# Kernel optimization log

Measured on AMD Instinct MI355X. Metric: run time of the kernel, lower is better.

## Reference

```python
import jax, jax.numpy as jnp
import numpy as np

N_NODES = 100000
N_EDGES = 1200000
N_HOP = 3
DIM = 64
EPS = 1e-5


def _bn(x):
    # BatchNorm1d over nodes, train-mode stats, gamma=1, beta=0
    m = x.mean(axis=0)
    v = x.var(axis=0)
    return (x - m) / jnp.sqrt(v + EPS)


def _gcn_conv(x, W, b, src, dst, n):
    # PyG GCNConv: add self-loops, symmetric deg^-1/2 (A+I) deg^-1/2, then bias
    xw = x @ W                                            # [N, D]
    deg = jax.ops.segment_sum(jnp.ones_like(src, dtype=xw.dtype), dst,
                              num_segments=n) + 1.0       # self-loop adds 1
    dinv = jax.lax.rsqrt(deg)                             # deg >= 1
    coef = dinv[src] * dinv[dst]                          # [E]
    agg = jax.ops.segment_sum(xw[src] * coef[:, None], dst, num_segments=n)
    agg = agg + (dinv * dinv)[:, None] * xw               # self-loop message
    return agg + b


def setup_inputs() -> dict:
    key = jax.random.key(0)
    ks = jax.random.split(key, 8)
    backbone_outputs = jax.random.normal(ks[0], (4, N_NODES, DIM), dtype=jnp.float32)
    khop_edge_index = jax.random.randint(ks[1], (N_HOP, 2, N_EDGES), 0, N_NODES)
    comb_w = jax.random.normal(ks[2], (N_HOP + 1, 3), dtype=jnp.float32)
    ego_W = jax.random.normal(ks[3], (DIM, DIM), dtype=jnp.float32) / np.sqrt(DIM)
    ego_b = jnp.zeros((DIM,), dtype=jnp.float32)
    conv_W = jax.random.normal(ks[4], (N_HOP, DIM, DIM), dtype=jnp.float32) / np.sqrt(DIM)
    conv_b = jnp.zeros((N_HOP, DIM), dtype=jnp.float32)
    return {"backbone_outputs": backbone_outputs, "comb_w": comb_w,
            "ego_W": ego_W, "ego_b": ego_b, "conv_W": conv_W, "conv_b": conv_b,
            "khop_edge_index": khop_edge_index}


def reference(backbone_outputs, comb_w, ego_W, ego_b, conv_W, conv_b, khop_edge_index):
    n = backbone_outputs.shape[1]
    # SimpleCombine: softmax-weighted mixes of backbone layer outputs (skip input)
    w = jax.nn.softmax(comb_w, axis=1)                    # [n_hop+1, 3]
    multi = jnp.einsum('ji,ind->jnd', w, backbone_outputs[1:])  # [n_hop+1, N, D]
    # ego path: linear -> BN (dropout=0)
    hidden = _bn(multi[0] @ ego_W + ego_b)
    for k in range(N_HOP):
        src = khop_edge_index[k, 0]
        dst = khop_edge_index[k, 1]
        prop = _gcn_conv(multi[k + 1], conv_W[k], conv_b[k], src, dst, n)
        hidden = hidden + jax.nn.relu(_bn(prop))
    return jax.nn.log_softmax(hidden, axis=1)
```

## Files before the change

### kernel.cpp

```cpp
#include <hip/hip_runtime.h>
#include <hip/hip_bf16.h>

#define NND 100000
#define NED 1200000
#define NHOP 3
#define DM 64
#define EPSV 1e-5f
#define NB1 391

typedef long long i64;
typedef unsigned short u16;
typedef unsigned int u32;

__device__ __forceinline__ float rlf(float v, int k) {
    return __builtin_bit_cast(float, __builtin_amdgcn_readlane(__builtin_bit_cast(int, v), k));
}
__device__ __forceinline__ float bf2f(u16 b) {
    return __builtin_bit_cast(float, (u32)b << 16);
}
__device__ __forceinline__ u16 f2bf(float f) {
    u32 u = __builtin_bit_cast(u32, f);
    return (u16)((u + 0x7FFFu + ((u >> 16) & 1u)) >> 16);
}

__global__ void k_weights(const float* __restrict__ comb_w, float* __restrict__ wsoft) {
    int j = threadIdx.x;
    if (j < NHOP + 1) {
        float a0 = comb_w[j * 3 + 0], a1 = comb_w[j * 3 + 1], a2 = comb_w[j * 3 + 2];
        float mx = fmaxf(a0, fmaxf(a1, a2));
        float e0 = expf(a0 - mx), e1 = expf(a1 - mx), e2 = expf(a2 - mx);
        float s = 1.0f / (e0 + e1 + e2);
        wsoft[j * 3 + 0] = e0 * s; wsoft[j * 3 + 1] = e1 * s; wsoft[j * 3 + 2] = e2 * s;
    }
}

__global__ __launch_bounds__(256) void k_gemm(const float* __restrict__ bb,
                                              const float* __restrict__ wsoft, int j,
                                              const float* __restrict__ W,
                                              const float* __restrict__ dinv, int scale,
                                              float* __restrict__ stats, int dostats,
                                              u16* __restrict__ xw) {
    const int lane = threadIdx.x & 63;
    float Wcol[DM];
#pragma unroll
    for (int k = 0; k < DM; k++) Wcol[k] = W[k * DM + lane];
    const float w0 = wsoft[j * 3 + 0], w1 = wsoft[j * 3 + 1], w2 = wsoft[j * 3 + 2];
    const float* b1 = bb + (i64)1 * NND * DM;
    const float* b2 = bb + (i64)2 * NND * DM;
    const float* b3 = bb + (i64)3 * NND * DM;
    int wave = (int)((blockIdx.x * blockDim.x + threadIdx.x) >> 6);
    int nw = (int)((gridDim.x * blockDim.x) >> 6);
    float s = 0.f, sq = 0.f;
    for (int n = wave; n < NND; n += nw) {
        i64 base = (i64)n * DM + lane;
        float m = w0 * b1[base] + w1 * b2[base] + w2 * b3[base];
        float a0 = 0.f, a1 = 0.f, a2 = 0.f, a3 = 0.f;
#pragma unroll
        for (int k = 0; k < DM; k += 4) {
            a0 = fmaf(rlf(m, k + 0), Wcol[k + 0], a0);
            a1 = fmaf(rlf(m, k + 1), Wcol[k + 1], a1);
            a2 = fmaf(rlf(m, k + 2), Wcol[k + 2], a2);
            a3 = fmaf(rlf(m, k + 3), Wcol[k + 3], a3);
        }
        float r = (a0 + a1) + (a2 + a3);
        if (scale) r *= dinv[n];
        xw[base] = f2bf(r);
        s += r; sq += r * r;
    }
    if (dostats) {
        __shared__ float ls[4][DM], lq[4][DM];
        int row = threadIdx.x >> 6;
        ls[row][lane] = s; lq[row][lane] = sq;
        __syncthreads();
        if (row == 0) {
            s  = ls[0][lane] + ls[1][lane] + ls[2][lane] + ls[3][lane];
            sq = lq[0][lane] + lq[1][lane] + lq[2][lane] + lq[3][lane];
            unsafeAtomicAdd(&stats[lane], s);
            unsafeAtomicAdd(&stats[DM + lane], sq);
        }
    }
}

__global__ __launch_bounds__(256) void k_deg(const int* __restrict__ dst, int* __restrict__ deg) {
    int i = blockIdx.x * blockDim.x + threadIdx.x;
    int stride = gridDim.x * blockDim.x;
    for (int e = i; e < NED; e += stride) atomicAdd(&deg[dst[e]], 1);
}

__global__ __launch_bounds__(256) void k_scan1(const int* __restrict__ deg,
                                               int* __restrict__ off,
                                               int* __restrict__ partials,
                                               float* __restrict__ dinv) {
    int t = threadIdx.x;
    int n = blockIdx.x * 256 + t;
    int d = (n < NND) ? deg[n] : 0;
    if (n < NND) dinv[n] = rsqrtf((float)d + 1.0f);
    __shared__ int sh[256];
    sh[t] = d;
    __syncthreads();
    for (int o = 1; o < 256; o <<= 1) {
        int v = (t >= o) ? sh[t - o] : 0;
        __syncthreads();
        sh[t] += v;
        __syncthreads();
    }
    if (n < NND) off[n] = sh[t] - d;
    if (t == 255) partials[blockIdx.x] = sh[255];
}

__global__ __launch_bounds__(512) void k_scan2(int* __restrict__ partials) {
    int t = threadIdx.x;
    int d = (t < NB1) ? partials[t] : 0;
    __shared__ int sh[512];
    sh[t] = d;
    __syncthreads();
    for (int o = 1; o < 512; o <<= 1) {
        int v = (t >= o) ? sh[t - o] : 0;
        __syncthreads();
        sh[t] += v;
        __syncthreads();
    }
    if (t < NB1) partials[t] = sh[t] - d;
}

__global__ __launch_bounds__(256) void k_bucket(const int* __restrict__ src,
                                                const int* __restrict__ dst,
                                                int* __restrict__ off,
                                                const int* __restrict__ partials,
                                                int* __restrict__ sortedsrc) {
    int i = blockIdx.x * blockDim.x + threadIdx.x;
    int stride = gridDim.x * blockDim.x;
    for (int e = i; e < NED; e += stride) {
        int d = dst[e];
        int pos = partials[d >> 8] + atomicAdd(&off[d], 1);
        sortedsrc[pos] = src[e];
    }
}

__global__ __launch_bounds__(256) void k_gather(const u16* __restrict__ xws,
                                                const int* __restrict__ sortedsrc,
                                                const int* __restrict__ off,
                                                const int* __restrict__ partials,
                                                const int* __restrict__ deg,
                                                const float* __restrict__ dinv,
                                                float* __restrict__ xbuf,
                                                float* __restrict__ stats) {
    const int lane = threadIdx.x & 63;
    int wave = (int)((blockIdx.x * blockDim.x + threadIdx.x) >> 6);
    int nw = (int)((gridDim.x * blockDim.x) >> 6);
    float s = 0.f, sq = 0.f;
    for (int n = wave; n < NND; n += nw) {
        int cnt = deg[n];
        int start = partials[n >> 8] + off[n] - cnt;
        float acc = bf2f(xws[(i64)n * DM + lane]);
        int i = 0;
        while (i < cnt) {
            int m = cnt - i; if (m > 64) m = 64;
            int sl = (lane < m) ? sortedsrc[start + i + lane] : 0;
            int t = 0;
            for (; t + 4 <= m; t += 4) {
                int s0 = __builtin_amdgcn_readlane(sl, t + 0);
                int s1 = __builtin_amdgcn_readlane(sl, t + 1);
                int s2 = __builtin_amdgcn_readlane(sl, t + 2);
                int s3 = __builtin_amdgcn_readlane(sl, t + 3);
                float v0 = bf2f(xws[(i64)s0 * DM + lane]);
                float v1 = bf2f(xws[(i64)s1 * DM + lane]);
                float v2 = bf2f(xws[(i64)s2 * DM + lane]);
                float v3 = bf2f(xws[(i64)s3 * DM + lane]);
                acc += ((v0 + v1) + (v2 + v3));
            }
            for (; t < m; t++) {
                int ss = __builtin_amdgcn_readlane(sl, t);
                acc += bf2f(xws[(i64)ss * DM + lane]);
            }
            i += m;
        }
        float x = acc * dinv[n];
        xbuf[(i64)n * DM + lane] = x;
        s += x; sq += x * x;
    }
    __shared__ float ls[4][DM], lq[4][DM];
    int row = threadIdx.x >> 6;
    ls[row][lane] = s; lq[row][lane] = sq;
    __syncthreads();
    if (row == 0) {
        s  = ls[0][lane] + ls[1][lane] + ls[2][lane] + ls[3][lane];
        sq = lq[0][lane] + lq[1][lane] + lq[2][lane] + lq[3][lane];
        unsafeAtomicAdd(&stats[lane], s);
        unsafeAtomicAdd(&stats[DM + lane], sq);
    }
}

__global__ __launch_bounds__(256) void k_apply(const float* __restrict__ xbuf,
                                               const u16* __restrict__ xwsA, int mode,
                                               const float* __restrict__ statsA,
                                               const float* __restrict__ statsB,
                                               float* __restrict__ hidden,
                                               float* __restrict__ out) {
    const int lane = threadIdx.x & 63;
    float meanB = statsB[lane] * (1.0f / NND);
    float varB = statsB[DM + lane] * (1.0f / NND) - meanB * meanB;
    float invB = rsqrtf(varB + EPSV);
    float meanA = 0.f, invA = 0.f;
    if (mode == 0) {
        meanA = statsA[lane] * (1.0f / NND);
        float varA = statsA[DM + lane] * (1.0f / NND) - meanA * meanA;
        invA = rsqrtf(varA + EPSV);
    }
    int wave = (int)((blockIdx.x * blockDim.x + threadIdx.x) >> 6);
    int nw = (int)((gridDim.x * blockDim.x) >> 6);
    for (int n = wave; n < NND; n += nw) {
        i64 i = (i64)n * DM + lane;
        float bn = (xbuf[i] - meanB) * invB;
        float r = fmaxf(bn, 0.0f);
        if (mode == 0) {
            hidden[i] = (bf2f(xwsA[i]) - meanA) * invA + r;
        } else if (mode == 1) {
            hidden[i] += r;
        } else {
            float h = hidden[i] + r;
            float mx = h;
#pragma unroll
            for (int o = 32; o >= 1; o >>= 1) mx = fmaxf(mx, __shfl_xor(mx, o));
            float e = expf(h - mx);
            float ssum = e;
#pragma unroll
            for (int o = 32; o >= 1; o >>= 1) ssum += __shfl_xor(ssum, o);
            out[i] = h - mx - logf(ssum);
        }
    }
}

extern "C" void kernel_launch(void* const* d_in, const int* in_sizes, int n_in,
                              void* d_out, int out_size, void* d_ws, size_t ws_size,
                              hipStream_t stream) {
    const float* bb     = (const float*)d_in[0];
    const float* comb_w = (const float*)d_in[1];
    const float* ego_W  = (const float*)d_in[2];
    const float* conv_W = (const float*)d_in[4];
    const int*   edges  = (const int*)d_in[6];
    float* out = (float*)d_out;

    const i64 NF = (i64)NND * DM;
    char* ws = (char*)d_ws;
    float* wsoft     = (float*)ws;
    float* stats     = wsoft + 64;
    u16*   xwsA      = (u16*)(stats + 512);
    u16*   xwsB      = xwsA + NF;
    float* xbuf      = (float*)(xwsB + NF);
    float* dinv      = xbuf + NF;
    int*   deg       = (int*)(dinv + NND);
    int*   off       = deg + NND;
    int*   partials  = off + NND;
    int*   sortedsrc = partials + 512;
    float* hidden = out;

    k_weights<<<1, 64, 0, stream>>>(comb_w, wsoft);
    hipMemsetAsync(stats, 0, 4 * 128 * sizeof(float), stream);

    k_gemm<<<1024, 256, 0, stream>>>(bb, wsoft, 0, ego_W, dinv, 0, stats, 1, xwsA);

    for (int k = 0; k < NHOP; k++) {
        const int* src = edges + (i64)k * 2 * NED;
        const int* dst = src + NED;
        float* statsB = stats + (k + 1) * 128;
        hipMemsetAsync(deg, 0, NND * sizeof(int), stream);
        k_deg<<<1024, 256, 0, stream>>>(dst, deg);
        k_scan1<<<NB1, 256, 0, stream>>>(deg, off, partials, dinv);
        k_scan2<<<1, 512, 0, stream>>>(partials);
        k_gemm<<<1024, 256, 0, stream>>>(bb, wsoft, k + 1, conv_W + (i64)k * DM * DM,
                                         dinv, 1, statsB, 0, xwsB);
        k_bucket<<<1024, 256, 0, stream>>>(src, dst, off, partials, sortedsrc);
        k_gather<<<4096, 256, 0, stream>>>(xwsB, sortedsrc, off, partials, deg, dinv,
                                           xbuf, statsB);
        k_apply<<<512, 256, 0, stream>>>(xbuf, xwsA, k, stats, statsB, hidden, out);
    }
}
```

Baseline: 1.087 ms.

## Batch CSR build across hops and vectorize bf16 gather with 8-lane groups

Builds the CSR for all three hops in one batch: a combined degree count, scan, rowptr finalize and bucket pass, instead of a separate sequence per hop. The softmax weights and the dinv scaling are now computed inline, which drops the weights kernel and the dinv array. The gather now loads each neighbor row as 16-byte uint4 bf16 vectors, with 8 groups of 8 lanes each handling a different neighbor, then reduces across groups with shuffles. The intermediate xbuf is stored in bf16 instead of fp32, which halves its traffic in the apply kernel at the cost of extra rounding before BatchNorm. Launch sizes are also changed.

```diff
diff --git a/kernel.cpp b/kernel.cpp
--- a/kernel.cpp
+++ b/kernel.cpp
@@ -22,29 +22,24 @@
     u32 u = __builtin_bit_cast(u32, f);
     return (u16)((u + 0x7FFFu + ((u >> 16) & 1u)) >> 16);
 }
-
-__global__ void k_weights(const float* __restrict__ comb_w, float* __restrict__ wsoft) {
-    int j = threadIdx.x;
-    if (j < NHOP + 1) {
-        float a0 = comb_w[j * 3 + 0], a1 = comb_w[j * 3 + 1], a2 = comb_w[j * 3 + 2];
-        float mx = fmaxf(a0, fmaxf(a1, a2));
-        float e0 = expf(a0 - mx), e1 = expf(a1 - mx), e2 = expf(a2 - mx);
-        float s = 1.0f / (e0 + e1 + e2);
-        wsoft[j * 3 + 0] = e0 * s; wsoft[j * 3 + 1] = e1 * s; wsoft[j * 3 + 2] = e2 * s;
-    }
-}
+__device__ __forceinline__ float lo_f(u32 w) { return __builtin_bit_cast(float, w << 16); }
+__device__ __forceinline__ float hi_f(u32 w) { return __builtin_bit_cast(float, w & 0xFFFF0000u); }
 
 __global__ __launch_bounds__(256) void k_gemm(const float* __restrict__ bb,
-                                              const float* __restrict__ wsoft, int j,
+                                              const float* __restrict__ comb_w, int j,
                                               const float* __restrict__ W,
-                                              const float* __restrict__ dinv, int scale,
+                                              const int* __restrict__ rowptr, int scale,
                                               float* __restrict__ stats, int dostats,
                                               u16* __restrict__ xw) {
     const int lane = threadIdx.x & 63;
     float Wcol[DM];
 #pragma unroll
     for (int k = 0; k < DM; k++) Wcol[k] = W[k * DM + lane];
-    const float w0 = wsoft[j * 3 + 0], w1 = wsoft[j * 3 + 1], w2 = wsoft[j * 3 + 2];
+    float c0 = comb_w[j * 3 + 0], c1 = comb_w[j * 3 + 1], c2 = comb_w[j * 3 + 2];
+    float mx = fmaxf(c0, fmaxf(c1, c2));
+    float e0 = expf(c0 - mx), e1 = expf(c1 - mx), e2 = expf(c2 - mx);
+    float es = 1.0f / (e0 + e1 + e2);
+    const float w0 = e0 * es, w1 = e1 * es, w2 = e2 * es;
     const float* b1 = bb + (i64)1 * NND * DM;
     const float* b2 = bb + (i64)2 * NND * DM;
     const float* b3 = bb + (i64)3 * NND * DM;
@@ -63,7 +58,10 @@
             a3 = fmaf(rlf(m, k + 3), Wcol[k + 3], a3);
         }
         float r = (a0 + a1) + (a2 + a3);
-        if (scale) r *= dinv[n];
+        if (scale) {
+            int rs = rowptr[n], re = rowptr[n + 1];
+            r *= rsqrtf((float)(re - rs) + 1.0f);
+        }
         xw[base] = f2bf(r);
         s += r; sq += r * r;
     }
@@ -81,20 +79,26 @@
     }
 }
 
-__global__ __launch_bounds__(256) void k_deg(const int* __restrict__ dst, int* __restrict__ deg) {
+__global__ __launch_bounds__(256) void k_deg3(const int* __restrict__ edges, int* __restrict__ deg) {
     int i = blockIdx.x * blockDim.x + threadIdx.x;
     int stride = gridDim.x * blockDim.x;
-    for (int e = i; e < NED; e += stride) atomicAdd(&deg[dst[e]], 1);
+    for (int e = i; e < NED; e += stride) {
+#pragma unroll
+        for (int h = 0; h < NHOP; h++) {
+            int d = edges[(i64)h * 2 * NED + NED + e];
+            atomicAdd(&deg[h * NND + d], 1);
+        }
+    }
 }
 
 __global__ __launch_bounds__(256) void k_scan1(const int* __restrict__ deg,
-                                               int* __restrict__ off,
-                                               int* __restrict__ partials,
-                                               float* __restrict__ dinv) {
+                                               int* __restrict__ loc,
+                                               int* __restrict__ partials) {
     int t = threadIdx.x;
-    int n = blockIdx.x * 256 + t;
-    int d = (n < NND) ? deg[n] : 0;
-    if (n < NND) dinv[n] = rsqrtf((float)d + 1.0f);
+    int h = blockIdx.x / NB1;
+    int lb = blockIdx.x - h * NB1;
+    int n = lb * 256 + t;
+    int d = (n < NND) ? deg[h * NND + n] : 0;
     __shared__ int sh[256];
     sh[t] = d;
     __syncthreads();
@@ -104,13 +108,14 @@
         sh[t] += v;
         __syncthreads();
     }
-    if (n < NND) off[n] = sh[t] - d;
-    if (t == 255) partials[blockIdx.x] = sh[255];
+    if (n < NND) loc[h * NND + n] = sh[t] - d;
+    if (t == 255) partials[h * 512 + lb] = sh[255];
 }
 
 __global__ __launch_bounds__(512) void k_scan2(int* __restrict__ partials) {
     int t = threadIdx.x;
-    int d = (t < NB1) ? partials[t] : 0;
+    int h = blockIdx.x;
+    int d = (t < NB1) ? partials[h * 512 + t] : 0;
     __shared__ int sh[512];
     sh[t] = d;
     __syncthreads();
@@ -120,78 +125,128 @@
         sh[t] += v;
         __syncthreads();
     }
-    if (t < NB1) partials[t] = sh[t] - d;
-}
-
-__global__ __launch_bounds__(256) void k_bucket(const int* __restrict__ src,
-                                                const int* __restrict__ dst,
-                                                int* __restrict__ off,
-                                                const int* __restrict__ partials,
-                                                int* __restrict__ sortedsrc) {
+    if (t < NB1) partials[h * 512 + t] = sh[t] - d;
+}
+
+__global__ __launch_bounds__(256) void k_fin(const int* __restrict__ loc,
+                                             const int* __restrict__ partials,
+                                             int* __restrict__ rowptr,
+                                             int* __restrict__ cursor) {
+    int i = blockIdx.x * blockDim.x + threadIdx.x;
+    if (i >= NHOP * (NND + 1)) return;
+    int h = i / (NND + 1);
+    int n = i - h * (NND + 1);
+    int v;
+    if (n == NND) v = NED;
+    else v = partials[h * 512 + (n >> 8)] + loc[h * NND + n];
+    rowptr[h * (NND + 1) + n] = v;
+    if (n < NND) cursor[h * NND + n] = v;
+}
+
+__global__ __launch_bounds__(256) void k_bucket3(const int* __restrict__ edges,
+                                                 int* __restrict__ cursor,
+                                                 int* __restrict__ sortedsrc) {
     int i = blockIdx.x * blockDim.x + threadIdx.x;
     int stride = gridDim.x * blockDim.x;
     for (int e = i; e < NED; e += stride) {
-        int d = dst[e];
-        int pos = partials[d >> 8] + atomicAdd(&off[d], 1);
-        sortedsrc[pos] = src[e];
+#pragma unroll
+        for (int h = 0; h < NHOP; h++) {
+            int s = edges[(i64)h * 2 * NED + e];
+            int d = edges[(i64)h * 2 * NED + NED + e];
+            int pos = atomicAdd(&cursor[h * NND + d], 1);
+            sortedsrc[(i64)h * NED + pos] = s;
+        }
     }
 }
 
 __global__ __launch_bounds__(256) void k_gather(const u16* __restrict__ xws,
-                                                const int* __restrict__ sortedsrc,
-                                                const int* __restrict__ off,
-                                                const int* __restrict__ partials,
-                                                const int* __restrict__ deg,
-                                                const float* __restrict__ dinv,
-                                                float* __restrict__ xbuf,
+                                                const int* __restrict__ sorted,
+                                                const int* __restrict__ rowptr,
+                                                u16* __restrict__ xbuf,
                                                 float* __restrict__ stats) {
     const int lane = threadIdx.x & 63;
+    const int g = lane >> 3;
+    const int c = lane & 7;
+    const int wv = threadIdx.x >> 6;
     int wave = (int)((blockIdx.x * blockDim.x + threadIdx.x) >> 6);
     int nw = (int)((gridDim.x * blockDim.x) >> 6);
-    float s = 0.f, sq = 0.f;
+    float sA[8] = {0,0,0,0,0,0,0,0}, qA[8] = {0,0,0,0,0,0,0,0};
     for (int n = wave; n < NND; n += nw) {
-        int cnt = deg[n];
-        int start = partials[n >> 8] + off[n] - cnt;
-        float acc = bf2f(xws[(i64)n * DM + lane]);
-        int i = 0;
-        while (i < cnt) {
-            int m = cnt - i; if (m > 64) m = 64;
-            int sl = (lane < m) ? sortedsrc[start + i + lane] : 0;
-            int t = 0;
-            for (; t + 4 <= m; t += 4) {
-                int s0 = __builtin_amdgcn_readlane(sl, t + 0);
-                int s1 = __builtin_amdgcn_readlane(sl, t + 1);
-                int s2 = __builtin_amdgcn_readlane(sl, t + 2);
-                int s3 = __builtin_amdgcn_readlane(sl, t + 3);
-                float v0 = bf2f(xws[(i64)s0 * DM + lane]);
-                float v1 = bf2f(xws[(i64)s1 * DM + lane]);
-                float v2 = bf2f(xws[(i64)s2 * DM + lane]);
-                float v3 = bf2f(xws[(i64)s3 * DM + lane]);
-                acc += ((v0 + v1) + (v2 + v3));
+        int start = rowptr[n];
+        int cnt = rowptr[n + 1] - start;
+        uint4 sv = *(const uint4*)(xws + (i64)n * DM + c * 8);
+        float selfw = (g == 0) ? 1.0f : 0.0f;
+        float acc[8];
+        acc[0] = lo_f(sv.x) * selfw; acc[1] = hi_f(sv.x) * selfw;
+        acc[2] = lo_f(sv.y) * selfw; acc[3] = hi_f(sv.y) * selfw;
+        acc[4] = lo_f(sv.z) * selfw; acc[5] = hi_f(sv.z) * selfw;
+        acc[6] = lo_f(sv.w) * selfw; acc[7] = hi_f(sv.w) * selfw;
+        int base = 0;
+        while (base < cnt) {
+            int take = cnt - base; if (take > 64) take = 64;
+            int eidx = start + base + lane;
+            if (eidx > NED - 1) eidx = NED - 1;
+            int sli = sorted[eidx];
+            int nr = (take + 7) >> 3;
+            for (int r = 0; r < nr; r += 2) {
+                int i0 = r * 8 + g;
+                int i1 = i0 + 8;
+                int s0 = __shfl(sli, i0);
+                int s1 = __shfl(sli, i1 & 63);
+                uint4 v0 = *(const uint4*)(xws + (i64)s0 * DM + c * 8);
+                uint4 v1 = *(const uint4*)(xws + (i64)s1 * DM + c * 8);
+                float m0 = (i0 < take) ? 1.0f : 0.0f;
+                float m1 = (i1 < take) ? 1.0f : 0.0f;
+                acc[0] = fmaf(lo_f(v0.x), m0, acc[0]); acc[1] = fmaf(hi_f(v0.x), m0, acc[1]);
+                acc[2] = fmaf(lo_f(v0.y), m0, acc[2]); acc[3] = fmaf(hi_f(v0.y), m0, acc[3]);
+                acc[4] = fmaf(lo_f(v0.z), m0, acc[4]); acc[5] = fmaf(hi_f(v0.z), m0, acc[5]);
+                acc[6] = fmaf(lo_f(v0.w), m0, acc[6]); acc[7] = fmaf(hi_f(v0.w), m0, acc[7]);
+                acc[0] = fmaf(lo_f(v1.x), m1, acc[0]); acc[1] = fmaf(hi_f(v1.x), m1, acc[1]);
+                acc[2] = fmaf(lo_f(v1.y), m1, acc[2]); acc[3] = fmaf(hi_f(v1.y), m1, acc[3]);
+                acc[4] = fmaf(lo_f(v1.z), m1, acc[4]); acc[5] = fmaf(hi_f(v1.z), m1, acc[5]);
+                acc[6] = fmaf(lo_f(v1.w), m1, acc[6]); acc[7] = fmaf(hi_f(v1.w), m1, acc[7]);
             }
-            for (; t < m; t++) {
-                int ss = __builtin_amdgcn_readlane(sl, t);
-                acc += bf2f(xws[(i64)ss * DM + lane]);
-            }
-            i += m;
-        }
-        float x = acc * dinv[n];
-        xbuf[(i64)n * DM + lane] = x;
-        s += x; sq += x * x;
-    }
-    __shared__ float ls[4][DM], lq[4][DM];
-    int row = threadIdx.x >> 6;
-    ls[row][lane] = s; lq[row][lane] = sq;
+            base += take;
+        }
+        float dinv = rsqrtf((float)cnt + 1.0f);
+#pragma unroll
+        for (int i = 0; i < 8; i++) {
+            float v = acc[i];
+            v += __shfl_xor(v, 8);
+            v += __shfl_xor(v, 16);
+            v += __shfl_xor(v, 32);
+            float x = v * dinv;
+            acc[i] = x;
+            sA[i] += x; qA[i] += x * x;
+        }
+        if (g == 0) {
+            uint4 o;
+            o.x = (u32)f2bf(acc[0]) | ((u32)f2bf(acc[1]) << 16);
+            o.y = (u32)f2bf(acc[2]) | ((u32)f2bf(acc[3]) << 16);
+            o.z = (u32)f2bf(acc[4]) | ((u32)f2bf(acc[5]) << 16);
+            o.w = (u32)f2bf(acc[6]) | ((u32)f2bf(acc[7]) << 16);
+            *(uint4*)(xbuf + (i64)n * DM + c * 8) = o;
+        }
+    }
+    __shared__ float red[2][4][DM];
+    if (g == 0) {
+#pragma unroll
+        for (int i = 0; i < 8; i++) {
+            red[0][wv][c * 8 + i] = sA[i];
+            red[1][wv][c * 8 + i] = qA[i];
+        }
+    }
     __syncthreads();
-    if (row == 0) {
-        s  = ls[0][lane] + ls[1][lane] + ls[2][lane] + ls[3][lane];
-        sq = lq[0][lane] + lq[1][lane] + lq[2][lane] + lq[3][lane];
-        unsafeAtomicAdd(&stats[lane], s);
-        unsafeAtomicAdd(&stats[DM + lane], sq);
-    }
-}
-
-__global__ __launch_bounds__(256) void k_apply(const float* __restrict__ xbuf,
+    if (threadIdx.x < DM) {
+        int f = threadIdx.x;
+        float s = red[0][0][f] + red[0][1][f] + red[0][2][f] + red[0][3][f];
+        float q = red[1][0][f] + red[1][1][f] + red[1][2][f] + red[1][3][f];
+        unsafeAtomicAdd(&stats[f], s);
+        unsafeAtomicAdd(&stats[DM + f], q);
+    }
+}
+
+__global__ __launch_bounds__(256) void k_apply(const u16* __restrict__ xbuf,
                                                const u16* __restrict__ xwsA, int mode,
                                                const float* __restrict__ statsA,
                                                const float* __restrict__ statsB,
@@ -211,7 +266,7 @@
     int nw = (int)((gridDim.x * blockDim.x) >> 6);
     for (int n = wave; n < NND; n += nw) {
         i64 i = (i64)n * DM + lane;
-        float bn = (xbuf[i] - meanB) * invB;
+        float bn = (bf2f(xbuf[i]) - meanB) * invB;
         float r = fmaxf(bn, 0.0f);
         if (mode == 0) {
             hidden[i] = (bf2f(xwsA[i]) - meanA) * invA + r;
@@ -243,36 +298,36 @@
 
     const i64 NF = (i64)NND * DM;
     char* ws = (char*)d_ws;
-    float* wsoft     = (float*)ws;
-    float* stats     = wsoft + 64;
-    u16*   xwsA      = (u16*)(stats + 512);
+    float* stats     = (float*)ws;
+    u16*   xwsA      = (u16*)(ws + 4096);
     u16*   xwsB      = xwsA + NF;
-    float* xbuf      = (float*)(xwsB + NF);
-    float* dinv      = xbuf + NF;
-    int*   deg       = (int*)(dinv + NND);
-    int*   off       = deg + NND;
-    int*   partials  = off + NND;
-    int*   sortedsrc = partials + 512;
+    u16*   xbuf      = xwsB + NF;
+    int*   deg       = (int*)(xbuf + NF);
+    int*   loc       = deg + 3 * NND;
+    int*   rowptr    = loc + 3 * NND;
+    int*   cursor    = rowptr + 3 * (NND + 1) + 64;
+    int*   partials  = cursor + 3 * NND;
+    int*   sortedsrc = partials + 3 * 512;
     float* hidden = out;
 
-    k_weights<<<1, 64, 0, stream>>>(comb_w, wsoft);
     hipMemsetAsync(stats, 0, 4 * 128 * sizeof(float), stream);
-
-    k_gemm<<<1024, 256, 0, stream>>>(bb, wsoft, 0, ego_W, dinv, 0, stats, 1, xwsA);
-
-    for (int k = 0; k < NHOP; k++) {
-        const int* src = edges + (i64)k * 2 * NED;
-        const int* dst = src + NED;
-        float* statsB = stats + (k + 1) * 128;
-        hipMemsetAsync(deg, 0, NND * sizeof(int), stream);
-        k_deg<<<1024, 256, 0, stream>>>(dst, deg);
-        k_scan1<<<NB1, 256, 0, stream>>>(deg, off, partials, dinv);
-        k_scan2<<<1, 512, 0, stream>>>(partials);
-        k_gemm<<<1024, 256, 0, stream>>>(bb, wsoft, k + 1, conv_W + (i64)k * DM * DM,
-                                         dinv, 1, statsB, 0, xwsB);
-        k_bucket<<<1024, 256, 0, stream>>>(src, dst, off, partials, sortedsrc);
-        k_gather<<<4096, 256, 0, stream>>>(xwsB, sortedsrc, off, partials, deg, dinv,
-                                           xbuf, statsB);
-        k_apply<<<512, 256, 0, stream>>>(xbuf, xwsA, k, stats, statsB, hidden, out);
-    }
-}
+    hipMemsetAsync(deg, 0, 3 * NND * sizeof(int), stream);
+
+    k_deg3<<<2048, 256, 0, stream>>>(edges, deg);
+    k_scan1<<<3 * NB1, 256, 0, stream>>>(deg, loc, partials);
+    k_scan2<<<3, 512, 0, stream>>>(partials);
+    k_fin<<<(3 * (NND + 1) + 255) / 256, 256, 0, stream>>>(loc, partials, rowptr, cursor);
+    k_bucket3<<<2048, 256, 0, stream>>>(edges, cursor, sortedsrc);
+
+    k_gemm<<<1024, 256, 0, stream>>>(bb, comb_w, 0, ego_W, rowptr, 0, stats, 1, xwsA);
+
+    for (int h = 0; h < NHOP; h++) {
+        const int* rp = rowptr + h * (NND + 1);
+        const int* ss = sortedsrc + (i64)h * NED;
+        float* statsB = stats + (h + 1) * 128;
+        k_gemm<<<1024, 256, 0, stream>>>(bb, comb_w, h + 1, conv_W + (i64)h * DM * DM,
+                                         rp, 1, statsB, 0, xwsB);
+        k_gather<<<6144, 256, 0, stream>>>(xwsB, ss, rp, xbuf, statsB);
+        k_apply<<<768, 256, 0, stream>>>(xbuf, xwsA, h, stats, statsB, hidden, out);
+    }
+}
```

Result: slower. 1.174 ms (+8.1%).
